# Performance work log

Measured on AMD Instinct MI355X. Metric: run time of the kernel, lower is better.

The kernel has to match this reference:

```python
import jax, jax.numpy as jnp
import numpy as np

MIN_K = 1024  # hard-negative mining floor per image (per_image=True branch)


def setup_inputs() -> dict:
    key = jax.random.key(0)
    k1, k2 = jax.random.split(key)
    B, C, D, H, W = 4, 3, 64, 256, 256
    inp = jax.random.normal(k1, (B, C, D, H, W), dtype=jnp.float32)
    tgt = jax.random.randint(k2, (B, D, H, W), 0, C, dtype=jnp.int64)
    return {"input": inp, "target": tgt}


def reference(input, target):
    b = input.shape[0]
    # per-pixel cross-entropy: -log_softmax over class dim, gathered at target
    logp = jax.nn.log_softmax(input, axis=1)                      # [B,C,D,H,W]
    ce = -jnp.take_along_axis(logp, target[:, None].astype(jnp.int32), axis=1)[:, 0]
    loss = ce.reshape(b, -1)                                      # [B, N]
    tflat = target.reshape(b, -1)                                 # [B, N]
    N = loss.shape[1]

    fg = tflat > 0                                                # [B, N]
    fg_num = fg.sum(axis=1)                                       # [B] int
    bg_num = N - fg_num                                           # [B] int
    k = jnp.minimum(bg_num, jnp.maximum(fg_num, MIN_K))           # [B] int

    # foreground term: mean of fg losses (0 if no fg)
    fg_sum = jnp.where(fg, loss, 0.0).sum(axis=1)                 # [B]
    fg_term = jnp.where(fg_num > 0,
                        fg_sum / jnp.maximum(fg_num, 1).astype(loss.dtype), 0.0)

    # background term: mean of top-k hardest bg losses (data-dependent k, fixed shapes)
    bg_masked = jnp.where(fg, -jnp.inf, loss)                     # fg -> -inf, never selected
    sorted_desc = -jnp.sort(-bg_masked, axis=1)                   # [B, N] descending
    sel = jnp.arange(N)[None, :] < k[:, None]                     # first k entries
    bg_sum = jnp.where(sel, sorted_desc, 0.0).sum(axis=1)         # [B]
    bg_term = jnp.where(bg_num > 0,
                        bg_sum / jnp.maximum(k, 1).astype(loss.dtype), 0.0)

    return jnp.sum(fg_term + bg_term) / b
```

## Files before the change

### kernel.cpp

```cpp
#include <hip/hip_runtime.h>

#define NPIX 4194304
#define BATCH 4
#define MINK 1024ULL
#define NBINS 4096
#define G1 1024

typedef unsigned long long u64;

__device__ __forceinline__ float pix_loss(float v0, float v1, float v2, int t) {
    float m = fmaxf(fmaxf(v0, v1), v2);
    float lse = m + __logf(__expf(v0 - m) + __expf(v1 - m) + __expf(v2 - m));
    float xt = (t == 0) ? v0 : ((t == 1) ? v1 : v2);
    return lse - xt;
}

__global__ __launch_bounds__(256) void k_reduce(const float* __restrict__ x,
                                                const int* __restrict__ tg,
                                                float* __restrict__ pfs,
                                                float* __restrict__ pbs,
                                                unsigned* __restrict__ pfc) {
    const int b = blockIdx.y;
    const float* xb = x + (size_t)b * 3 * NPIX;
    const int* tb = tg + (size_t)b * NPIX;
    float fs = 0.f, bs = 0.f;
    int fc = 0;
    const int stride = G1 * 256 * 4;
#pragma unroll
    for (int it = 0; it < NPIX / stride; ++it) {
        const int i = it * stride + (blockIdx.x * 256 + threadIdx.x) * 4;
        const float4 a = *(const float4*)(xb + i);
        const float4 c = *(const float4*)(xb + NPIX + i);
        const float4 d = *(const float4*)(xb + 2 * NPIX + i);
        const int4 t4 = *(const int4*)(tb + i);
        float l;
        l = pix_loss(a.x, c.x, d.x, t4.x); if (t4.x > 0) { fs += l; fc++; } else bs += l;
        l = pix_loss(a.y, c.y, d.y, t4.y); if (t4.y > 0) { fs += l; fc++; } else bs += l;
        l = pix_loss(a.z, c.z, d.z, t4.z); if (t4.z > 0) { fs += l; fc++; } else bs += l;
        l = pix_loss(a.w, c.w, d.w, t4.w); if (t4.w > 0) { fs += l; fc++; } else bs += l;
    }
#pragma unroll
    for (int off = 32; off > 0; off >>= 1) {
        fs += __shfl_down(fs, off);
        bs += __shfl_down(bs, off);
        fc += __shfl_down(fc, off);
    }
    __shared__ float sfs[4], sbs[4];
    __shared__ int sfc[4];
    const int wid = threadIdx.x >> 6;
    if ((threadIdx.x & 63) == 0) { sfs[wid] = fs; sbs[wid] = bs; sfc[wid] = fc; }
    __syncthreads();
    if (threadIdx.x == 0) {
        const int slot = b * G1 + blockIdx.x;
        pfs[slot] = sfs[0] + sfs[1] + sfs[2] + sfs[3];
        pbs[slot] = sbs[0] + sbs[1] + sbs[2] + sbs[3];
        pfc[slot] = (unsigned)(sfc[0] + sfc[1] + sfc[2] + sfc[3]);
    }
}

__global__ __launch_bounds__(256) void k_sum(const float* __restrict__ pfs,
                                             const float* __restrict__ pbs,
                                             const unsigned* __restrict__ pfc,
                                             double* __restrict__ fg_sum,
                                             double* __restrict__ bg_sum,
                                             u64* __restrict__ fg_cnt,
                                             unsigned* __restrict__ hist_cnt,
                                             float* __restrict__ hist_sum,
                                             int have_hist) {
    __shared__ double sd0[4], sd1[4];
    __shared__ u64 sc[4];
    for (int b = 0; b < BATCH; ++b) {
        double fs = 0.0, bs = 0.0;
        u64 fc = 0;
        for (int i = threadIdx.x; i < G1; i += 256) {
            fs += (double)pfs[b * G1 + i];
            bs += (double)pbs[b * G1 + i];
            fc += (u64)pfc[b * G1 + i];
        }
#pragma unroll
        for (int off = 32; off > 0; off >>= 1) {
            fs += __shfl_down(fs, off);
            bs += __shfl_down(bs, off);
            fc += __shfl_down(fc, off);
        }
        const int wid = threadIdx.x >> 6;
        if ((threadIdx.x & 63) == 0) { sd0[wid] = fs; sd1[wid] = bs; sc[wid] = fc; }
        __syncthreads();
        if (threadIdx.x == 0) {
            fg_sum[b] = sd0[0] + sd0[1] + sd0[2] + sd0[3];
            bg_sum[b] = sd1[0] + sd1[1] + sd1[2] + sd1[3];
            fg_cnt[b] = sc[0] + sc[1] + sc[2] + sc[3];
        }
        __syncthreads();
    }
    if (have_hist) {
        for (int i = threadIdx.x; i < BATCH * NBINS; i += 256) {
            hist_cnt[i] = 0u;
            hist_sum[i] = 0.f;
        }
    }
}

__global__ __launch_bounds__(256) void k_hist(const float* __restrict__ x,
                                              const int* __restrict__ tg,
                                              const u64* __restrict__ fg_cnt,
                                              unsigned int* __restrict__ hist_cnt,
                                              float* __restrict__ hist_sum) {
    const int b = blockIdx.y;
    const u64 fc = fg_cnt[b];
    const u64 bg = (u64)NPIX - fc;
    u64 mk = fc > MINK ? fc : MINK;
    const u64 k = bg < mk ? bg : mk;
    if (k >= bg) return;

    __shared__ unsigned int hc[NBINS];
    __shared__ float hs[NBINS];
    for (int i = threadIdx.x; i < NBINS; i += blockDim.x) { hc[i] = 0u; hs[i] = 0.f; }
    __syncthreads();

    const float* xb = x + (size_t)b * 3 * NPIX;
    const int* tb = tg + (size_t)b * NPIX;
    const int stride = gridDim.x * blockDim.x * 4;
    for (int i = (blockIdx.x * blockDim.x + threadIdx.x) * 4; i < NPIX; i += stride) {
        const float4 a = *(const float4*)(xb + i);
        const float4 c = *(const float4*)(xb + NPIX + i);
        const float4 d = *(const float4*)(xb + 2 * NPIX + i);
        const int4 t4 = *(const int4*)(tb + i);
        float v[4][3] = {{a.x, c.x, d.x}, {a.y, c.y, d.y}, {a.z, c.z, d.z}, {a.w, c.w, d.w}};
        int tt[4] = {t4.x, t4.y, t4.z, t4.w};
#pragma unroll
        for (int j = 0; j < 4; ++j) {
            if (tt[j] == 0) {
                float l = fmaxf(pix_loss(v[j][0], v[j][1], v[j][2], tt[j]), 0.f);
                unsigned bin = __float_as_uint(l) >> 20;
                atomicAdd(&hc[bin], 1u);
                atomicAdd(&hs[bin], l);
            }
        }
    }
    __syncthreads();
    for (int i = threadIdx.x; i < NBINS; i += blockDim.x) {
        if (hc[i]) {
            atomicAdd(&hist_cnt[(size_t)b * NBINS + i], hc[i]);
            atomicAdd(&hist_sum[(size_t)b * NBINS + i], hs[i]);
        }
    }
}

__global__ void k_final(const double* __restrict__ fg_sum,
                        const double* __restrict__ bg_sum,
                        const u64* __restrict__ fg_cnt,
                        const unsigned int* __restrict__ hist_cnt,
                        const float* __restrict__ hist_sum,
                        int have_hist, float* __restrict__ out) {
    if (threadIdx.x != 0 || blockIdx.x != 0) return;
    double acc = 0.0;
    for (int b = 0; b < BATCH; ++b) {
        const u64 fc = fg_cnt[b];
        const u64 bg = (u64)NPIX - fc;
        u64 mk = fc > MINK ? fc : MINK;
        const u64 k = bg < mk ? bg : mk;
        double fg_term = (fc > 0) ? fg_sum[b] / (double)fc : 0.0;
        double bg_topk;
        if (k >= bg || !have_hist) {
            bg_topk = bg_sum[b];
        } else {
            u64 cnt = 0;
            double s = 0.0;
            bg_topk = 0.0;
            for (int i = NBINS - 1; i >= 0; --i) {
                unsigned c = hist_cnt[(size_t)b * NBINS + i];
                if (cnt + c >= k) {
                    double edge = (double)__uint_as_float(((unsigned)i) << 20);
                    bg_topk = s + (double)(k - cnt) * edge;
                    break;
                }
                cnt += c;
                s += (double)hist_sum[(size_t)b * NBINS + i];
            }
        }
        u64 kd = k > 1 ? k : 1;
        double bg_term = (bg > 0) ? bg_topk / (double)kd : 0.0;
        acc += fg_term + bg_term;
    }
    out[0] = (float)(acc / (double)BATCH);
}

extern "C" void kernel_launch(void* const* d_in, const int* in_sizes, int n_in,
                              void* d_out, int out_size, void* d_ws, size_t ws_size,
                              hipStream_t stream) {
    const float* x = (const float*)d_in[0];
    const int* tg = (const int*)d_in[1];
    float* out = (float*)d_out;

    char* ws = (char*)d_ws;
    float* pfs = (float*)ws;
    float* pbs = (float*)(ws + 16384);
    unsigned* pfc = (unsigned*)(ws + 32768);
    double* fg_sum = (double*)(ws + 49152);
    double* bg_sum = (double*)(ws + 49184);
    u64* fg_cnt = (u64*)(ws + 49216);
    unsigned* hist_cnt = (unsigned*)(ws + 49280);
    float* hist_sum = (float*)(ws + 49280 + (size_t)BATCH * NBINS * 4);
    const size_t need = 49280 + (size_t)BATCH * NBINS * 8;
    const int have_hist = (ws_size >= need) ? 1 : 0;

    dim3 block(256);
    dim3 grid1(G1, BATCH);
    k_reduce<<<grid1, block, 0, stream>>>(x, tg, pfs, pbs, pfc);
    k_sum<<<1, block, 0, stream>>>(pfs, pbs, pfc, fg_sum, bg_sum, fg_cnt,
                                   hist_cnt, hist_sum, have_hist);
    if (have_hist) {
        dim3 hgrid(1024, BATCH);
        k_hist<<<hgrid, block, 0, stream>>>(x, tg, fg_cnt, hist_cnt, hist_sum);
    }
    k_final<<<1, 64, 0, stream>>>(fg_sum, bg_sum, fg_cnt, hist_cnt, hist_sum, have_hist, out);
}
```

Before: 61.41 us.

## Fuse final reduction into sum kernel and last-block histogram scan

Folds the final top-k/average computation into the single-block sum kernel, which writes the output directly and sets a flag marking which images need the histogram. The histogram kernel reads the flag, exits early if unneeded, and otherwise performs the final scan in the last-arriving block via an atomic counter. This removes one kernel launch and shrinks the histogram grid, at the cost of cross-block fence/atomic synchronization.

```diff
diff --git a/kernel.cpp b/kernel.cpp
--- a/kernel.cpp
+++ b/kernel.cpp
@@ -5,6 +5,7 @@
 #define MINK 1024ULL
 #define NBINS 4096
 #define G1 1024
+#define HG 256
 
 typedef unsigned long long u64;
 
@@ -58,17 +59,21 @@
     }
 }
 
-__global__ __launch_bounds__(256) void k_sum(const float* __restrict__ pfs,
-                                             const float* __restrict__ pbs,
-                                             const unsigned* __restrict__ pfc,
-                                             double* __restrict__ fg_sum,
-                                             double* __restrict__ bg_sum,
-                                             u64* __restrict__ fg_cnt,
-                                             unsigned* __restrict__ hist_cnt,
-                                             float* __restrict__ hist_sum,
-                                             int have_hist) {
+__global__ __launch_bounds__(256) void k_sumfin(const float* __restrict__ pfs,
+                                                const float* __restrict__ pbs,
+                                                const unsigned* __restrict__ pfc,
+                                                double* __restrict__ fg_sum,
+                                                double* __restrict__ bg_sum,
+                                                u64* __restrict__ fg_cnt,
+                                                unsigned* __restrict__ hist_cnt,
+                                                float* __restrict__ hist_sum,
+                                                unsigned* __restrict__ flags,
+                                                float* __restrict__ out,
+                                                int have_hist) {
     __shared__ double sd0[4], sd1[4];
     __shared__ u64 sc[4];
+    __shared__ double tfs[BATCH], tbs[BATCH];
+    __shared__ u64 tfc[BATCH];
     for (int b = 0; b < BATCH; ++b) {
         double fs = 0.0, bs = 0.0;
         u64 fc = 0;
@@ -87,103 +92,150 @@
         if ((threadIdx.x & 63) == 0) { sd0[wid] = fs; sd1[wid] = bs; sc[wid] = fc; }
         __syncthreads();
         if (threadIdx.x == 0) {
-            fg_sum[b] = sd0[0] + sd0[1] + sd0[2] + sd0[3];
-            bg_sum[b] = sd1[0] + sd1[1] + sd1[2] + sd1[3];
-            fg_cnt[b] = sc[0] + sc[1] + sc[2] + sc[3];
-        }
-        __syncthreads();
+            tfs[b] = sd0[0] + sd0[1] + sd0[2] + sd0[3];
+            tbs[b] = sd1[0] + sd1[1] + sd1[2] + sd1[3];
+            tfc[b] = sc[0] + sc[1] + sc[2] + sc[3];
+            fg_sum[b] = tfs[b];
+            bg_sum[b] = tbs[b];
+            fg_cnt[b] = tfc[b];
+        }
+        __syncthreads();
+    }
+    if (threadIdx.x == 0) {
+        double acc = 0.0;
+        unsigned need = 0u;
+        for (int b = 0; b < BATCH; ++b) {
+            const u64 fc = tfc[b];
+            const u64 bg = (u64)NPIX - fc;
+            u64 mk = fc > MINK ? fc : MINK;
+            const u64 k = bg < mk ? bg : mk;
+            double fg_term = (fc > 0) ? tfs[b] / (double)fc : 0.0;
+            u64 kd = k > 1 ? k : 1;
+            double bg_term = (bg > 0) ? tbs[b] / (double)kd : 0.0;
+            if (k < bg && have_hist) need |= (1u << b);
+            acc += fg_term + bg_term;
+        }
+        out[0] = (float)(acc / (double)BATCH);
+        flags[0] = need;
+        flags[1] = 0u;
     }
     if (have_hist) {
-        for (int i = threadIdx.x; i < BATCH * NBINS; i += 256) {
-            hist_cnt[i] = 0u;
-            hist_sum[i] = 0.f;
+        uint4 z4 = make_uint4(0u, 0u, 0u, 0u);
+        uint4* hc4 = (uint4*)hist_cnt;
+        uint4* hs4 = (uint4*)hist_sum;
+        for (int i = threadIdx.x; i < BATCH * NBINS / 4; i += 256) {
+            hc4[i] = z4;
+            hs4[i] = z4;
         }
     }
 }
 
 __global__ __launch_bounds__(256) void k_hist(const float* __restrict__ x,
                                               const int* __restrict__ tg,
+                                              const double* __restrict__ fg_sum,
+                                              const double* __restrict__ bg_sum,
                                               const u64* __restrict__ fg_cnt,
-                                              unsigned int* __restrict__ hist_cnt,
-                                              float* __restrict__ hist_sum) {
+                                              unsigned* __restrict__ hist_cnt,
+                                              float* __restrict__ hist_sum,
+                                              unsigned* __restrict__ flags,
+                                              float* __restrict__ out) {
+    const unsigned need = flags[0];
+    if (need == 0u) return;
+
     const int b = blockIdx.y;
-    const u64 fc = fg_cnt[b];
-    const u64 bg = (u64)NPIX - fc;
-    u64 mk = fc > MINK ? fc : MINK;
-    const u64 k = bg < mk ? bg : mk;
-    if (k >= bg) return;
-
-    __shared__ unsigned int hc[NBINS];
+    __shared__ unsigned hc[NBINS];
     __shared__ float hs[NBINS];
-    for (int i = threadIdx.x; i < NBINS; i += blockDim.x) { hc[i] = 0u; hs[i] = 0.f; }
+
+    if (need & (1u << b)) {
+        for (int i = threadIdx.x; i < NBINS; i += 256) { hc[i] = 0u; hs[i] = 0.f; }
+        __syncthreads();
+        const float* xb = x + (size_t)b * 3 * NPIX;
+        const int* tb = tg + (size_t)b * NPIX;
+        const int stride = HG * 256 * 4;
+        for (int i = (blockIdx.x * 256 + threadIdx.x) * 4; i < NPIX; i += stride) {
+            const float4 a = *(const float4*)(xb + i);
+            const float4 c = *(const float4*)(xb + NPIX + i);
+            const float4 d = *(const float4*)(xb + 2 * NPIX + i);
+            const int4 t4 = *(const int4*)(tb + i);
+            float v[4][3] = {{a.x, c.x, d.x}, {a.y, c.y, d.y}, {a.z, c.z, d.z}, {a.w, c.w, d.w}};
+            int tt[4] = {t4.x, t4.y, t4.z, t4.w};
+#pragma unroll
+            for (int j = 0; j < 4; ++j) {
+                if (tt[j] == 0) {
+                    float l = fmaxf(pix_loss(v[j][0], v[j][1], v[j][2], tt[j]), 0.f);
+                    unsigned bin = __float_as_uint(l) >> 20;
+                    atomicAdd(&hc[bin], 1u);
+                    atomicAdd(&hs[bin], l);
+                }
+            }
+        }
+        __syncthreads();
+        for (int i = threadIdx.x; i < NBINS; i += 256) {
+            if (hc[i]) {
+                atomicAdd(&hist_cnt[(size_t)b * NBINS + i], hc[i]);
+                atomicAdd(&hist_sum[(size_t)b * NBINS + i], hs[i]);
+            }
+        }
+    }
+
+    __threadfence();
     __syncthreads();
-
-    const float* xb = x + (size_t)b * 3 * NPIX;
-    const int* tb = tg + (size_t)b * NPIX;
-    const int stride = gridDim.x * blockDim.x * 4;
-    for (int i = (blockIdx.x * blockDim.x + threadIdx.x) * 4; i < NPIX; i += stride) {
-        const float4 a = *(const float4*)(xb + i);
-        const float4 c = *(const float4*)(xb + NPIX + i);
-        const float4 d = *(const float4*)(xb + 2 * NPIX + i);
-        const int4 t4 = *(const int4*)(tb + i);
-        float v[4][3] = {{a.x, c.x, d.x}, {a.y, c.y, d.y}, {a.z, c.z, d.z}, {a.w, c.w, d.w}};
-        int tt[4] = {t4.x, t4.y, t4.z, t4.w};
-#pragma unroll
-        for (int j = 0; j < 4; ++j) {
-            if (tt[j] == 0) {
-                float l = fmaxf(pix_loss(v[j][0], v[j][1], v[j][2], tt[j]), 0.f);
-                unsigned bin = __float_as_uint(l) >> 20;
-                atomicAdd(&hc[bin], 1u);
-                atomicAdd(&hs[bin], l);
-            }
-        }
+    __shared__ int is_last;
+    if (threadIdx.x == 0) {
+        unsigned v = atomicAdd(&flags[1], 1u);
+        is_last = (v == (unsigned)(HG * BATCH) - 1u) ? 1 : 0;
     }
     __syncthreads();
-    for (int i = threadIdx.x; i < NBINS; i += blockDim.x) {
-        if (hc[i]) {
-            atomicAdd(&hist_cnt[(size_t)b * NBINS + i], hc[i]);
-            atomicAdd(&hist_sum[(size_t)b * NBINS + i], hs[i]);
-        }
-    }
-}
-
-__global__ void k_final(const double* __restrict__ fg_sum,
-                        const double* __restrict__ bg_sum,
-                        const u64* __restrict__ fg_cnt,
-                        const unsigned int* __restrict__ hist_cnt,
-                        const float* __restrict__ hist_sum,
-                        int have_hist, float* __restrict__ out) {
-    if (threadIdx.x != 0 || blockIdx.x != 0) return;
-    double acc = 0.0;
-    for (int b = 0; b < BATCH; ++b) {
-        const u64 fc = fg_cnt[b];
-        const u64 bg = (u64)NPIX - fc;
-        u64 mk = fc > MINK ? fc : MINK;
-        const u64 k = bg < mk ? bg : mk;
-        double fg_term = (fc > 0) ? fg_sum[b] / (double)fc : 0.0;
-        double bg_topk;
-        if (k >= bg || !have_hist) {
-            bg_topk = bg_sum[b];
-        } else {
-            u64 cnt = 0;
-            double s = 0.0;
-            bg_topk = 0.0;
-            for (int i = NBINS - 1; i >= 0; --i) {
-                unsigned c = hist_cnt[(size_t)b * NBINS + i];
-                if (cnt + c >= k) {
-                    double edge = (double)__uint_as_float(((unsigned)i) << 20);
-                    bg_topk = s + (double)(k - cnt) * edge;
-                    break;
+    if (!is_last) return;
+
+    __threadfence();
+    __shared__ double sbt[BATCH];
+    for (int b2 = 0; b2 < BATCH; ++b2) {
+        if (need & (1u << b2)) {
+            for (int i = threadIdx.x; i < NBINS; i += 256) {
+                hc[i] = __hip_atomic_load(&hist_cnt[(size_t)b2 * NBINS + i],
+                                          __ATOMIC_ACQUIRE, __HIP_MEMORY_SCOPE_AGENT);
+                hs[i] = __hip_atomic_load(&hist_sum[(size_t)b2 * NBINS + i],
+                                          __ATOMIC_ACQUIRE, __HIP_MEMORY_SCOPE_AGENT);
+            }
+            __syncthreads();
+            if (threadIdx.x == 0) {
+                const u64 fc = fg_cnt[b2];
+                const u64 bg = (u64)NPIX - fc;
+                u64 mk = fc > MINK ? fc : MINK;
+                const u64 k = bg < mk ? bg : mk;
+                u64 cnt = 0;
+                double s = 0.0, bg_topk = 0.0;
+                for (int i = NBINS - 1; i >= 0; --i) {
+                    unsigned c = hc[i];
+                    if (cnt + c >= k) {
+                        double edge = (double)__uint_as_float(((unsigned)i) << 20);
+                        bg_topk = s + (double)(k - cnt) * edge;
+                        break;
+                    }
+                    cnt += c;
+                    s += (double)hs[i];
                 }
-                cnt += c;
-                s += (double)hist_sum[(size_t)b * NBINS + i];
-            }
-        }
-        u64 kd = k > 1 ? k : 1;
-        double bg_term = (bg > 0) ? bg_topk / (double)kd : 0.0;
-        acc += fg_term + bg_term;
-    }
-    out[0] = (float)(acc / (double)BATCH);
+                sbt[b2] = bg_topk;
+            }
+            __syncthreads();
+        }
+    }
+    if (threadIdx.x == 0) {
+        double acc = 0.0;
+        for (int b2 = 0; b2 < BATCH; ++b2) {
+            const u64 fc = fg_cnt[b2];
+            const u64 bg = (u64)NPIX - fc;
+            u64 mk = fc > MINK ? fc : MINK;
+            const u64 k = bg < mk ? bg : mk;
+            double fg_term = (fc > 0) ? fg_sum[b2] / (double)fc : 0.0;
+            double bg_topk = (need & (1u << b2)) ? sbt[b2] : bg_sum[b2];
+            u64 kd = k > 1 ? k : 1;
+            double bg_term = (bg > 0) ? bg_topk / (double)kd : 0.0;
+            acc += fg_term + bg_term;
+        }
+        out[0] = (float)(acc / (double)BATCH);
+    }
 }
 
 extern "C" void kernel_launch(void* const* d_in, const int* in_sizes, int n_in,
@@ -200,19 +252,20 @@
     double* fg_sum = (double*)(ws + 49152);
     double* bg_sum = (double*)(ws + 49184);
     u64* fg_cnt = (u64*)(ws + 49216);
+    unsigned* flags = (unsigned*)(ws + 49248);
     unsigned* hist_cnt = (unsigned*)(ws + 49280);
     float* hist_sum = (float*)(ws + 49280 + (size_t)BATCH * NBINS * 4);
-    const size_t need = 49280 + (size_t)BATCH * NBINS * 8;
-    const int have_hist = (ws_size >= need) ? 1 : 0;
+    const size_t need_ws = 49280 + (size_t)BATCH * NBINS * 8;
+    const int have_hist = (ws_size >= need_ws) ? 1 : 0;
 
     dim3 block(256);
     dim3 grid1(G1, BATCH);
     k_reduce<<<grid1, block, 0, stream>>>(x, tg, pfs, pbs, pfc);
-    k_sum<<<1, block, 0, stream>>>(pfs, pbs, pfc, fg_sum, bg_sum, fg_cnt,
-                                   hist_cnt, hist_sum, have_hist);
+    k_sumfin<<<1, block, 0, stream>>>(pfs, pbs, pfc, fg_sum, bg_sum, fg_cnt,
+                                      hist_cnt, hist_sum, flags, out, have_hist);
     if (have_hist) {
-        dim3 hgrid(1024, BATCH);
-        k_hist<<<hgrid, block, 0, stream>>>(x, tg, fg_cnt, hist_cnt, hist_sum);
-    }
-    k_final<<<1, 64, 0, stream>>>(fg_sum, bg_sum, fg_cnt, hist_cnt, hist_sum, have_hist, out);
-}
+        dim3 hgrid(HG, BATCH);
+        k_hist<<<hgrid, block, 0, stream>>>(x, tg, fg_sum, bg_sum, fg_cnt,
+                                            hist_cnt, hist_sum, flags, out);
+    }
+}
```

After: 58.07 us. 1.06x faster.
